# Performance work log

Hardware: AMD Instinct MI355X
Metric: run time of the kernel (lower is better)

The kernel has to match this reference:

```python
import jax, jax.numpy as jnp
import numpy as np

B, S, D = 4, 2048, 1024
H = 16
HD = D // H  # head_dim = 64


def setup_inputs() -> dict:
    key = jax.random.key(0)
    ks = jax.random.split(key, 5)
    scale = 1.0 / np.sqrt(D)
    return {
        "x": jax.random.normal(ks[0], (B, S, D), dtype=jnp.float32),
        "Wq": jax.random.normal(ks[1], (D, D), dtype=jnp.float32) * scale,
        "Wk": jax.random.normal(ks[2], (D, D), dtype=jnp.float32) * scale,
        "Wv": jax.random.normal(ks[3], (D, D), dtype=jnp.float32) * scale,
        "Wo": jax.random.normal(ks[4], (D, D), dtype=jnp.float32) * scale,
        "bo": jnp.zeros((D,), dtype=jnp.float32),
    }


def reference(x, Wq, Wk, Wv, Wo, bo):
    b, s, d = x.shape
    # project and split heads: [b, h, s, hd]
    q = (x @ Wq).reshape(b, s, H, HD).transpose(0, 2, 1, 3)
    k = (x @ Wk).reshape(b, s, H, HD).transpose(0, 2, 1, 3)
    v = (x @ Wv).reshape(b, s, H, HD).transpose(0, 2, 1, 3)
    # scores: [b, h, s, s]
    scores = jnp.einsum("bhqd,bhkd->bhqk", q, k)
    # NOTE: original uses tril(diagonal=1) -> allows one future token (off-by-one)
    mask = jnp.tril(jnp.ones((s, s), dtype=bool), k=1)
    scores = jnp.where(mask, scores, -jnp.inf)
    attn = jax.nn.softmax(scores / np.sqrt(HD), axis=-1)
    # dropout p=0.0 (deterministic baseline): identity
    ctx = jnp.einsum("bhqk,bhkd->bhqd", attn, v)
    ctx = ctx.transpose(0, 2, 1, 3).reshape(b, s, d)
    return ctx @ Wo + bo
```

## Files before the change

### kernel.cpp

```cpp
#include <hip/hip_runtime.h>
#include <hip/hip_bf16.h>

#define Bq 4
#define Sq 2048
#define Dq 1024
#define Hq 16
#define HDq 64
#define Mq (Bq*Sq)

typedef unsigned short u16;
typedef __attribute__((ext_vector_type(8))) __bf16 b16x8;
typedef __attribute__((ext_vector_type(4))) float f32x4;
typedef __attribute__((ext_vector_type(4))) unsigned int u32x4;

__device__ inline float bf2f(u16 h){ union{unsigned u; float f;} v; v.u = ((unsigned)h)<<16; return v.f; }
__device__ inline u16 f2bf(float f){ union{float f; unsigned u;} v; v.f=f; unsigned r = v.u + 0x7FFFu + ((v.u>>16)&1u); return (u16)(r>>16); }
__device__ inline u16 truncbf(float f){ union{float f; unsigned u;} v; v.f=f; return (u16)(v.u>>16); }
__device__ inline float ld_elem(const void* p, size_t i, int isf32){
  return isf32 ? ((const float*)p)[i] : bf2f(((const u16*)p)[i]);
}
__device__ inline void ld16(const u16* g, u16* l){
  __builtin_amdgcn_global_load_lds((const __attribute__((address_space(1))) void*)g,
                                   (__attribute__((address_space(3))) void*)l, 16, 0, 0);
}

#if __has_builtin(__builtin_amdgcn_exp2f)
#define EXP2(x) __builtin_amdgcn_exp2f(x)
#else
#define EXP2(x) __expf((x)*0.69314718056f)
#endif
#define SCALE_LOG2E 0.18033688011112042f

__device__ inline int detect_wave(const unsigned* __restrict__ x, int t){
  unsigned w = x[t & 255];
  unsigned long long m1 = __ballot(((w>>7)&0xFFu)>=0x90u);
  unsigned long long m2 = __ballot(((w>>23)&0xFFu)>=0x90u);
  return (__popcll(m1)+__popcll(m2)) > 8 ? 1 : 0;
}

__global__ __launch_bounds__(256) void prep(
    const void* __restrict__ x,
    const void* __restrict__ W0, const void* __restrict__ W1,
    const void* __restrict__ W2, const void* __restrict__ W3,
    u16* __restrict__ xc,
    u16* __restrict__ T0, u16* __restrict__ T1,
    u16* __restrict__ T2, u16* __restrict__ T3){
  __shared__ u16 tile[64][65];
  const int t = threadIdx.x;
  const int f = detect_wave((const unsigned*)x, t);
  const int bid = blockIdx.x;
  if (bid < 4096){
    int i = (bid*256 + t)*8;
    if(f){
      const float* xf=(const float*)x;
      #pragma unroll
      for(int j=0;j<8;j++) xc[i+j] = f2bf(xf[i+j]);
    } else {
      *(u32x4*)&xc[i] = *(const u32x4*)((const u16*)x + i);
    }
  } else {
    int idx = bid - 4096;
    int z = idx >> 8, rem = idx & 255;
    int k0 = (rem & 15)*64, n0 = (rem >> 4)*64;
    const void* src = (z==0)?W0:(z==1)?W1:(z==2)?W2:W3;
    u16*       dst = (z==0)?T0:(z==1)?T1:(z==2)?T2:T3;
    #pragma unroll
    for(int r=0;r<16;r++){
      int row = r*4 + (t>>6), col = t&63;
      tile[row][col] = f2bf(ld_elem(src, (size_t)(k0+row)*Dq + n0 + col, f));
    }
    __syncthreads();
    #pragma unroll
    for(int r=0;r<16;r++){
      int row = r*4 + (t>>6), col = t&63;
      dst[(size_t)(n0+row)*Dq + k0 + col] = tile[col][row];
    }
  }
}

template<int MODE>
__global__ __launch_bounds__(256, 3) void gemm2p(
    const u16* __restrict__ A, const u16* __restrict__ Bt,
    u16* __restrict__ O0, u16* __restrict__ O1, u16* __restrict__ O2,
    void* __restrict__ Og, const void* __restrict__ bias,
    const unsigned* __restrict__ xdet){
  constexpr int NT = Dq/32;
  __shared__ u16 Asl[3][128*32];
  __shared__ u16 Bsl[3][128*32];
  const int f = (MODE==1) ? detect_wave(xdet, threadIdx.x) : 0;
  const int t = threadIdx.x;
  const int lane = t & 63, wave = t >> 6;
  const int quad = lane >> 4, l16 = lane & 15;
  const int wr = wave >> 1, wc = wave & 1;
  int L = blockIdx.x + blockIdx.y*gridDim.x;
  int k8 = L & 7, ii = L >> 3;
  int m0, n0;
  if (MODE==0){
    int nsb = ii >> 6, rem = ii & 63;
    int mg = rem >> 3, ng = rem & 7;
    m0 = (k8*8 + mg)*128; n0 = (nsb*8 + ng)*128;
  } else {
    int mg = ii >> 3, ng = ii & 7;
    m0 = (k8*8 + mg)*128; n0 = ng*128;
  }

  f32x4 acc[4][4] = {};

  auto stageA = [&](int T, int s){
    #pragma unroll
    for(int r=0;r<2;r++){
      int idx = t + (r<<8);
      int row = idx>>2, g = idx&3;
      int gl = g ^ ((row>>1)&3);
      ld16(&A[(size_t)(m0+row)*Dq + (T<<5) + gl*8], &Asl[s][idx*8]);
    }
  };
  auto stageB = [&](int T, int s){
    #pragma unroll
    for(int r=0;r<2;r++){
      int idx = t + (r<<8);
      int row = idx>>2, g = idx&3;
      int gl = g ^ ((row>>1)&3);
      ld16(&Bt[(size_t)(n0+row)*Dq + (T<<5) + gl*8], &Bsl[s][idx*8]);
    }
  };
  auto ldA = [&](int s, int i)->b16x8{
    int row = wr*64 + i*16 + l16;
    return *(const b16x8*)&Asl[s][row*32 + ((quad ^ ((row>>1)&3))<<3)];
  };
  auto ldB = [&](int s, int j)->b16x8{
    int row = wc*64 + j*16 + l16;
    return *(const b16x8*)&Bsl[s][row*32 + ((quad ^ ((row>>1)&3))<<3)];
  };
  #define MFMA_BF16 __builtin_amdgcn_mfma_f32_16x16x32_bf16

  stageA(0,0); stageB(0,0); stageA(1,1); stageB(1,1);
  asm volatile("s_waitcnt vmcnt(4)" ::: "memory");
  __builtin_amdgcn_s_barrier();
  __builtin_amdgcn_sched_barrier(0);

  int s0=0, s1=1, s2=2;
  for(int tt=0; tt<NT; ++tt){
    if(tt+2<NT){ stageA(tt+2, s2); stageB(tt+2, s2); }
    b16x8 af[4], bf[4];
    #pragma unroll
    for(int i=0;i<4;i++) af[i]=ldA(s0,i);
    #pragma unroll
    for(int j=0;j<4;j++) bf[j]=ldB(s0,j);
    asm volatile("s_waitcnt lgkmcnt(0)" ::: "memory");
    __builtin_amdgcn_sched_barrier(0);
    __builtin_amdgcn_s_setprio(1);
    #pragma unroll
    for(int i=0;i<4;i++)
      #pragma unroll
      for(int j=0;j<4;j++)
        acc[i][j]=MFMA_BF16(af[i],bf[j],acc[i][j],0,0,0);
    __builtin_amdgcn_s_setprio(0);
    if(tt<NT-2) asm volatile("s_waitcnt vmcnt(4)" ::: "memory");
    else        asm volatile("s_waitcnt vmcnt(0)" ::: "memory");
    __builtin_amdgcn_s_barrier();
    __builtin_amdgcn_sched_barrier(0);
    int x2=s0; s0=s1; s1=s2; s2=x2;
  }

  #pragma unroll
  for(int i=0;i<4;i++){
    #pragma unroll
    for(int j=0;j<4;j++){
      int n = n0 + wc*64 + j*16 + l16;
      #pragma unroll
      for(int r=0;r<4;r++){
        int m = m0 + wr*64 + i*16 + quad*4 + r;
        float c = acc[i][j][r];
        if (MODE==1){
          float c2 = c + ld_elem(bias, n, f);
          if (f) ((float*)Og)[(size_t)m*Dq + n] = c2;
          else   ((u16*)Og)[(size_t)m*Dq + n]   = f2bf(c2);
        } else {
          int z = n >> 10, nn2 = n & 1023;
          int b = m >> 11, s2x = m & 2047;
          int h = nn2 >> 6, hd = nn2 & 63;
          if (z==0)      O0[(((size_t)(b*Hq + h))*Sq + s2x)*HDq + hd] = f2bf(c*SCALE_LOG2E);
          else if (z==1) O1[(((size_t)(b*Hq + h))*Sq + s2x)*HDq + hd] = f2bf(c);
          else           O2[(((size_t)(b*Hq + h))*HDq + hd)*Sq + s2x] = f2bf(c);
        }
      }
    }
  }
  #undef MFMA_BF16
}

__global__ __launch_bounds__(256) void flash_attn(
    const u16* __restrict__ Q, const u16* __restrict__ K,
    const u16* __restrict__ VT, u16* __restrict__ C){
  __shared__ u16 Kt[128*64];
  __shared__ u16 Vt[64*128];
  __shared__ u16 Pl[4][16][72];
  const int t = threadIdx.x;
  const int lane = t&63, wave = t>>6, quad = lane>>4, l16 = lane&15;
  int L  = blockIdx.x + blockIdx.y*gridDim.x;
  int k8 = L & 7, ii = L >> 3;
  const int bh = k8*8 + (ii>>3);
  const int p  = ii & 7;
  const int b = bh >> 4, h = bh & 15;
  const int qt[4] = { p, 15-p, 16+p, 31-p };
  int nk[4];
  #pragma unroll
  for(int tt=0;tt<4;tt++){ int v = qt[tt]+2; nk[tt] = (v<32)?v:32; }
  const int nrounds = (nk[3]+1)>>1;
  const u16* Qh = Q  + (size_t)bh*Sq*HDq;
  const u16* Kh = K  + (size_t)bh*Sq*HDq;
  const u16* Vh = VT + (size_t)bh*HDq*Sq;

  b16x8 aq[4][2];
  #pragma unroll
  for(int tt=0;tt<4;tt++){
    const u16* qp = Qh + (size_t)(qt[tt]*64 + wave*16 + l16)*HDq + quad*8;
    aq[tt][0] = *(const b16x8*)qp;
    aq[tt][1] = *(const b16x8*)(qp + 32);
  }
  b16x8 vone;
  #pragma unroll
  for(int i=0;i<8;i++) vone[i] = (__bf16)1.0f;

  const f32x4 fzero = {0.f,0.f,0.f,0.f};
  f32x4 Oa[4][4]; f32x4 lacc[4];
  #pragma unroll
  for(int tt=0;tt<4;tt++){ lacc[tt]=fzero; for(int j=0;j<4;j++) Oa[tt][j]=fzero; }

  for(int kt2=0; kt2<nrounds; kt2++){
    __syncthreads();
    #pragma unroll
    for(int r=0;r<4;r++){
      int idx = t + (r<<8);
      int row = idx>>3, g = idx&7;
      int csw = (g ^ (row&7))<<3;
      ld16(Kh + (size_t)(kt2*128+row)*HDq + csw, Kt + idx*8);
    }
    #pragma unroll
    for(int r=0;r<4;r++){
      int idx = t + (r<<8);
      int row = idx>>4, g = idx&15;
      int csw = (g ^ (row&15))<<3;
      ld16(Vh + (size_t)row*Sq + (size_t)kt2*128 + csw, Vt + idx*8);
    }
    __syncthreads();

    #pragma unroll
    for(int half=0; half<2; half++){
      const int kt = kt2*2 + half;
      #pragma unroll
      for(int tt=0;tt<4;tt++){
        if (kt >= nk[tt]) continue;
        const int qq0 = qt[tt]*64;
        f32x4 sc[4];
        #pragma unroll
        for(int jn=0;jn<4;jn++){
          int krow = half*64 + jn*16 + l16;
          const u16* kp = &Kt[krow*64];
          f32x4 s = fzero;
          b16x8 bk0 = *(const b16x8*)&kp[((quad     ^ (krow&7))<<3)];
          b16x8 bk1 = *(const b16x8*)&kp[(((quad+4) ^ (krow&7))<<3)];
          s = __builtin_amdgcn_mfma_f32_16x16x32_bf16(aq[tt][0], bk0, s, 0,0,0);
          s = __builtin_amdgcn_mfma_f32_16x16x32_bf16(aq[tt][1], bk1, s, 0,0,0);
          sc[jn] = s;
        }
        if (kt < qt[tt]) {
          #pragma unroll
          for(int jn=0;jn<4;jn++)
            #pragma unroll
            for(int r=0;r<4;r++)
              Pl[wave][quad*4+r][jn*16+l16] = truncbf(EXP2(sc[jn][r]));
        } else {
          const int qbase = qq0 + wave*16 + quad*4;
          #pragma unroll
          for(int jn=0;jn<4;jn++){
            int kg = kt*64 + jn*16 + l16;
            #pragma unroll
            for(int r=0;r<4;r++){
              float sv = sc[jn][r];
              if (kg > qbase + r + 1) sv = -__builtin_inff();
              Pl[wave][quad*4+r][jn*16+l16] = truncbf(EXP2(sv));
            }
          }
        }
        #pragma unroll
        for(int ks=0;ks<2;ks++){
          b16x8 ap = *(const b16x8*)&Pl[wave][l16][ks*32 + quad*8];
          int glog = half*8 + ks*4 + quad;
          #pragma unroll
          for(int jd=0;jd<4;jd++){
            int hd = jd*16 + l16;
            b16x8 bv = *(const b16x8*)&Vt[hd*128 + ((glog ^ (hd&15))<<3)];
            Oa[tt][jd] = __builtin_amdgcn_mfma_f32_16x16x32_bf16(ap, bv, Oa[tt][jd], 0,0,0);
          }
          lacc[tt] = __builtin_amdgcn_mfma_f32_16x16x32_bf16(ap, vone, lacc[tt], 0,0,0);
        }
      }
    }
  }
  #pragma unroll
  for(int tt=0;tt<4;tt++){
    const int qq0 = qt[tt]*64;
    #pragma unroll
    for(int r=0;r<4;r++){
      int s = qq0 + wave*16 + quad*4 + r;
      float inv = 1.0f / lacc[tt][r];
      #pragma unroll
      for(int jd=0;jd<4;jd++)
        C[((size_t)(b*Sq + s))*Dq + h*HDq + jd*16 + l16] = f2bf(Oa[tt][jd][r]*inv);
    }
  }
}

extern "C" void kernel_launch(void* const* d_in, const int* in_sizes, int n_in,
                              void* d_out, int out_size, void* d_ws, size_t ws_size,
                              hipStream_t stream){
  const void* x  = d_in[0];
  const void* Wq = d_in[1];
  const void* Wk = d_in[2];
  const void* Wv = d_in[3];
  const void* Wo = d_in[4];
  const void* bo = d_in[5];

  char* ws = (char*)d_ws;
  size_t off = 0;
  auto wsalloc = [&](size_t bytes)->void*{
    void* p = ws + off; off += (bytes + 255) & ~(size_t)255; return p;
  };
  u16* WqT = (u16*)wsalloc((size_t)Dq*Dq*2);
  u16* WkT = (u16*)wsalloc((size_t)Dq*Dq*2);
  u16* WvT = (u16*)wsalloc((size_t)Dq*Dq*2);
  u16* WoT = (u16*)wsalloc((size_t)Dq*Dq*2);
  u16* xc  = (u16*)wsalloc((size_t)Mq*Dq*2);
  u16* Qb  = (u16*)wsalloc((size_t)Mq*Dq*2);
  u16* Kb  = (u16*)wsalloc((size_t)Mq*Dq*2);
  u16* VTb = (u16*)wsalloc((size_t)Mq*Dq*2);
  u16* Cb  = (u16*)wsalloc((size_t)Mq*Dq*2);

  prep<<<dim3(5120), 256, 0, stream>>>(x, Wq,Wk,Wv,Wo, xc, WqT,WkT,WvT,WoT);
  gemm2p<0><<<dim3(24, 64), 256, 0, stream>>>(xc, WqT, Qb,Kb,VTb, nullptr, nullptr, nullptr);
  flash_attn<<<dim3(8, Bq*Hq), 256, 0, stream>>>(Qb, Kb, VTb, Cb);
  gemm2p<1><<<dim3(8, 64), 256, 0, stream>>>(Cb, WoT, nullptr,nullptr,nullptr, d_out, bo, (const unsigned*)x);
}
```

Measured before the change: 193.9 us.

## Replace direct global-to-LDS triple buffering with register-staged double buffering

The GEMM main loop stops using global_load_lds into three shared-memory stages. It now loads each tile into registers and writes them to one of two LDS buffers, with the global load issued two tiles ahead. This cuts LDS use per block, which may allow more resident blocks, and moves the store to LDS under program control. In exchange it adds VGPR pressure and explicit ds_write instructions, and each iteration waits vmcnt(0) before writing LDS, which can expose global-load latency.

```diff
diff --git a/kernel.cpp b/kernel.cpp
--- a/kernel.cpp
+++ b/kernel.cpp
@@ -85,8 +85,8 @@
     void* __restrict__ Og, const void* __restrict__ bias,
     const unsigned* __restrict__ xdet){
   constexpr int NT = Dq/32;
-  __shared__ u16 Asl[3][128*32];
-  __shared__ u16 Bsl[3][128*32];
+  __shared__ u16 Asl[2][128*32];
+  __shared__ u16 Bsl[2][128*32];
   const int f = (MODE==1) ? detect_wave(xdet, threadIdx.x) : 0;
   const int t = threadIdx.x;
   const int lane = t & 63, wave = t >> 6;
@@ -105,23 +105,24 @@
   }
 
   f32x4 acc[4][4] = {};
-
-  auto stageA = [&](int T, int s){
+  u32x4 rg[4];
+
+  auto loadG = [&](int T){
     #pragma unroll
     for(int r=0;r<2;r++){
       int idx = t + (r<<8);
       int row = idx>>2, g = idx&3;
       int gl = g ^ ((row>>1)&3);
-      ld16(&A[(size_t)(m0+row)*Dq + (T<<5) + gl*8], &Asl[s][idx*8]);
-    }
-  };
-  auto stageB = [&](int T, int s){
+      rg[r]   = *(const u32x4*)&A [(size_t)(m0+row)*Dq + (T<<5) + gl*8];
+      rg[2+r] = *(const u32x4*)&Bt[(size_t)(n0+row)*Dq + (T<<5) + gl*8];
+    }
+  };
+  auto writeL = [&](int s){
     #pragma unroll
     for(int r=0;r<2;r++){
       int idx = t + (r<<8);
-      int row = idx>>2, g = idx&3;
-      int gl = g ^ ((row>>1)&3);
-      ld16(&Bt[(size_t)(n0+row)*Dq + (T<<5) + gl*8], &Bsl[s][idx*8]);
+      *(u32x4*)&Asl[s][idx*8] = rg[r];
+      *(u32x4*)&Bsl[s][idx*8] = rg[2+r];
     }
   };
   auto ldA = [&](int s, int i)->b16x8{
@@ -134,19 +135,26 @@
   };
   #define MFMA_BF16 __builtin_amdgcn_mfma_f32_16x16x32_bf16
 
-  stageA(0,0); stageB(0,0); stageA(1,1); stageB(1,1);
-  asm volatile("s_waitcnt vmcnt(4)" ::: "memory");
+  loadG(0);
+  asm volatile("s_waitcnt vmcnt(0)" ::: "memory");
+  writeL(0);
+  loadG(1);
+  asm volatile("s_waitcnt lgkmcnt(0)" ::: "memory");
   __builtin_amdgcn_s_barrier();
   __builtin_amdgcn_sched_barrier(0);
 
-  int s0=0, s1=1, s2=2;
   for(int tt=0; tt<NT; ++tt){
-    if(tt+2<NT){ stageA(tt+2, s2); stageB(tt+2, s2); }
+    const int s = tt&1;
+    if(tt+1<NT){
+      asm volatile("s_waitcnt vmcnt(0)" ::: "memory");
+      writeL(s^1);
+    }
+    if(tt+2<NT) loadG(tt+2);
     b16x8 af[4], bf[4];
     #pragma unroll
-    for(int i=0;i<4;i++) af[i]=ldA(s0,i);
-    #pragma unroll
-    for(int j=0;j<4;j++) bf[j]=ldB(s0,j);
+    for(int i=0;i<4;i++) af[i]=ldA(s,i);
+    #pragma unroll
+    for(int j=0;j<4;j++) bf[j]=ldB(s,j);
     asm volatile("s_waitcnt lgkmcnt(0)" ::: "memory");
     __builtin_amdgcn_sched_barrier(0);
     __builtin_amdgcn_s_setprio(1);
@@ -156,11 +164,8 @@
       for(int j=0;j<4;j++)
         acc[i][j]=MFMA_BF16(af[i],bf[j],acc[i][j],0,0,0);
     __builtin_amdgcn_s_setprio(0);
-    if(tt<NT-2) asm volatile("s_waitcnt vmcnt(4)" ::: "memory");
-    else        asm volatile("s_waitcnt vmcnt(0)" ::: "memory");
     __builtin_amdgcn_s_barrier();
     __builtin_amdgcn_sched_barrier(0);
-    int x2=s0; s0=s1; s1=s2; s2=x2;
   }
 
   #pragma unroll
```

Measured after the change: 191.5 us. About the same (-1.3%).
